# Kernel tuning notes

Measured on AMD Instinct MI355X. Metric: run time of the kernel, lower is better.

Reference implementation:

```python
import jax, jax.numpy as jnp
import numpy as np

B, T, C = 2, 2048, 1024
N_HEAD = 16
HEAD_DIM = C // N_HEAD


def setup_inputs() -> dict:
    key = jax.random.key(0)
    k1, k2, k3 = jax.random.split(key, 3)
    x = jax.random.normal(k1, (B, T, C), dtype=jnp.float32)
    # weights stored as [in, out]; torch Linear computes x @ W.T with weight [out, in]
    W_qkv = jax.random.normal(k2, (C, 3 * C), dtype=jnp.float32) * (1.0 / np.sqrt(C))
    W_proj = jax.random.normal(k3, (C, C), dtype=jnp.float32) * (1.0 / np.sqrt(C))
    return {"x": x, "W_qkv": W_qkv, "W_proj": W_proj}


def reference(x, W_qkv, W_proj):
    Bb, Tt, Cc = x.shape
    qkv = x @ W_qkv                                # [B,T,3C]
    q, k, v = jnp.split(qkv, 3, axis=2)
    # [B,T,H,D] -> [B,H,T,D]
    q = q.reshape(Bb, Tt, N_HEAD, HEAD_DIM).transpose(0, 2, 1, 3)
    k = k.reshape(Bb, Tt, N_HEAD, HEAD_DIM).transpose(0, 2, 1, 3)
    v = v.reshape(Bb, Tt, N_HEAD, HEAD_DIM).transpose(0, 2, 1, 3)
    scale = 1.0 / np.sqrt(HEAD_DIM).astype(np.float32)
    att = jnp.einsum('bhqd,bhkd->bhqk', q, k) * scale   # [B,H,T,T]
    causal = jnp.tril(jnp.ones((Tt, Tt), dtype=bool))
    att = jnp.where(causal[None, None], att, -jnp.inf)
    att = jax.nn.softmax(att, axis=-1)
    y = jnp.einsum('bhqk,bhkd->bhqd', att, v)           # [B,H,T,D]
    y = y.transpose(0, 2, 1, 3).reshape(Bb, Tt, Cc)
    return y @ W_proj
```

## Files before the change

kernel.cpp:

```cpp
#include <hip/hip_runtime.h>
#include <hip/hip_bf16.h>
#include <math.h>


typedef __bf16 bf16_t;
typedef __bf16 bf16x4 __attribute__((ext_vector_type(4)));
typedef __bf16 bf16x8 __attribute__((ext_vector_type(8)));
typedef float  f32x4  __attribute__((ext_vector_type(4)));

#define MFMA16(a, b, c) __builtin_amdgcn_mfma_f32_16x16x32_bf16((a), (b), (c), 0, 0, 0)

#define Bn 2
#define Tn 2048
#define Cn 1024
#define Hn 16
#define Dn 64
#define C3 3072
#define Mn 4096
#define QKW 2048
#define NEG_BIG (-1e30f)
#define SCL2 0.18033688011112042f
#define M2   17.31234049066756f

__device__ __forceinline__ void gload_lds16(const void* g, void* l) {
    __builtin_amdgcn_global_load_lds(
        (const __attribute__((address_space(1))) unsigned int*)g,
        (__attribute__((address_space(3))) unsigned int*)l, 16, 0, 0);
}

__global__ __launch_bounds__(256) void transpose_cvt(const float* __restrict__ in,
                                                     bf16_t* __restrict__ out,
                                                     int K, int N) {
    __shared__ float tile[32][33];
    int n0 = blockIdx.x * 32, k0 = blockIdx.y * 32;
    int tx = threadIdx.x, ty = threadIdx.y;
#pragma unroll
    for (int i = 0; i < 32; i += 8)
        tile[ty + i][tx] = in[(size_t)(k0 + ty + i) * N + n0 + tx];
    __syncthreads();
#pragma unroll
    for (int i = 0; i < 32; i += 8)
        out[(size_t)(n0 + ty + i) * K + k0 + tx] = (bf16_t)tile[tx][ty + i];
}

__global__ __launch_bounds__(256) void cvt_bf16(const float* __restrict__ in,
                                                bf16_t* __restrict__ out) {
    size_t i = ((size_t)blockIdx.x * 256 + threadIdx.x) * 8;
    f32x4 a = *(const f32x4*)(in + i);
    f32x4 b = *(const f32x4*)(in + i + 4);
    bf16x8 r;
    r[0] = (bf16_t)a[0]; r[1] = (bf16_t)a[1]; r[2] = (bf16_t)a[2]; r[3] = (bf16_t)a[3];
    r[4] = (bf16_t)b[0]; r[5] = (bf16_t)b[1]; r[6] = (bf16_t)b[2]; r[7] = (bf16_t)b[3];
    *(bf16x8*)(out + i) = r;
}

template <typename AT, typename CT, int MODE>
__global__ __launch_bounds__(256) void gemm_m97(const AT* __restrict__ A, int lda,
                                                const bf16_t* __restrict__ BT,
                                                CT* __restrict__ Cout, int ldc, int Kd,
                                                bf16_t* __restrict__ qk,
                                                bf16_t* __restrict__ vT) {
    constexpr bool AF32 = (sizeof(AT) == 4);
    __shared__ AT     As[128 * 32];
    __shared__ bf16_t Bs[128 * 32];

    const int tid = threadIdx.x;
    const int w = tid >> 6, lane = tid & 63;
    const int l16 = lane & 15, quad = lane >> 4;
    const int wm = w & 1, wn = w >> 1;
    const int n0 = blockIdx.x * 128;
    const int m0 = blockIdx.y * 128;

    f32x4 zero = {0.f, 0.f, 0.f, 0.f};
    f32x4 acc[4][4];
#pragma unroll
    for (int mb = 0; mb < 4; mb++)
#pragma unroll
        for (int nb = 0; nb < 4; nb++) acc[mb][nb] = zero;

    for (int k = 0; k < Kd; k += 32) {
        __syncthreads();
        if (AF32) {
#pragma unroll
            for (int j = 0; j < 4; j++) {
                int seg = w * 4 + j;
                int r = seg * 8 + (lane >> 3);
                int cc = (lane & 7) ^ (r & 7);
                const float* g = (const float*)A + (size_t)(m0 + r) * lda + k + cc * 4;
                gload_lds16(g, (char*)As + seg * 1024);
            }
        } else {
#pragma unroll
            for (int j = 0; j < 2; j++) {
                int seg = w * 2 + j;
                int r = seg * 16 + (lane >> 2);
                int cc = (lane & 3) ^ (r & 3);
                const bf16_t* g = (const bf16_t*)A + (size_t)(m0 + r) * lda + k + cc * 8;
                gload_lds16(g, (char*)As + seg * 1024);
            }
        }
#pragma unroll
        for (int j = 0; j < 2; j++) {
            int seg = w * 2 + j;
            int r = seg * 16 + (lane >> 2);
            int cc = (lane & 3) ^ (r & 3);
            const bf16_t* g = BT + (size_t)(n0 + r) * Kd + k + cc * 8;
            gload_lds16(g, (char*)Bs + seg * 1024);
        }
        __syncthreads();

        bf16x8 af[4], bf[4];
#pragma unroll
        for (int mb = 0; mb < 4; mb++) {
            int r = wm * 64 + mb * 16 + l16;
            if (AF32) {
                f32x4 x0 = *(const f32x4*)((const char*)As + (r * 8 + ((quad * 2) ^ (r & 7))) * 16);
                f32x4 x1 = *(const f32x4*)((const char*)As + (r * 8 + ((quad * 2 + 1) ^ (r & 7))) * 16);
                bf16x8 t;
                t[0] = (bf16_t)x0[0]; t[1] = (bf16_t)x0[1]; t[2] = (bf16_t)x0[2]; t[3] = (bf16_t)x0[3];
                t[4] = (bf16_t)x1[0]; t[5] = (bf16_t)x1[1]; t[6] = (bf16_t)x1[2]; t[7] = (bf16_t)x1[3];
                af[mb] = t;
            } else {
                af[mb] = *(const bf16x8*)((const char*)As + (r * 4 + (quad ^ (r & 3))) * 16);
            }
        }
#pragma unroll
        for (int nb = 0; nb < 4; nb++) {
            int r = wn * 64 + nb * 16 + l16;
            bf[nb] = *(const bf16x8*)((const char*)Bs + (r * 4 + (quad ^ (r & 3))) * 16);
        }
#pragma unroll
        for (int mb = 0; mb < 4; mb++)
#pragma unroll
            for (int nb = 0; nb < 4; nb++)
                acc[mb][nb] = MFMA16(af[mb], bf[nb], acc[mb][nb]);
    }

#pragma unroll
    for (int mb = 0; mb < 4; mb++)
#pragma unroll
        for (int nb = 0; nb < 4; nb++) {
            const int col = n0 + wn * 64 + nb * 16 + l16;
            const int row0 = m0 + wm * 64 + mb * 16 + quad * 4;
            if (MODE == 0) {
#pragma unroll
                for (int rr = 0; rr < 4; rr++)
                    Cout[(size_t)(row0 + rr) * ldc + col] = (CT)acc[mb][nb][rr];
            } else {
                if (col < 2048) {
#pragma unroll
                    for (int rr = 0; rr < 4; rr++)
                        qk[(size_t)(row0 + rr) * QKW + col] = (bf16_t)acc[mb][nb][rr];
                } else {
                    int hcol = col - 2048;
                    int bb = row0 >> 11, t0 = row0 & 2047;
                    bf16x4 pv;
#pragma unroll
                    for (int rr = 0; rr < 4; rr++) pv[rr] = (bf16_t)acc[mb][nb][rr];
                    *(bf16x4*)(vT + ((size_t)(bb * 1024 + hcol)) * Tn + t0) = pv;
                }
            }
        }
}

__global__ __launch_bounds__(256) void gemm_s(const bf16_t* __restrict__ A, int lda,
                                              const bf16_t* __restrict__ BT,
                                              float* __restrict__ Cout, int ldc, int Kd) {
    __shared__ bf16_t As[64 * 32];
    __shared__ bf16_t Bs[128 * 32];

    const int tid = threadIdx.x;
    const int w = tid >> 6, lane = tid & 63;
    const int l16 = lane & 15, quad = lane >> 4;
    const int wm = w & 1, wn = w >> 1;
    const int n0 = blockIdx.x * 128;
    const int m0 = blockIdx.y * 64;

    f32x4 zero = {0.f, 0.f, 0.f, 0.f};
    f32x4 acc[2][4];
#pragma unroll
    for (int mb = 0; mb < 2; mb++)
#pragma unroll
        for (int nb = 0; nb < 4; nb++) acc[mb][nb] = zero;

    for (int k = 0; k < Kd; k += 32) {
        __syncthreads();
        {
            int r = w * 16 + (lane >> 2);
            int cc = (lane & 3) ^ (r & 3);
            const bf16_t* g = A + (size_t)(m0 + r) * lda + k + cc * 8;
            gload_lds16(g, (char*)As + w * 1024);
        }
#pragma unroll
        for (int j = 0; j < 2; j++) {
            int seg = w * 2 + j;
            int r = seg * 16 + (lane >> 2);
            int cc = (lane & 3) ^ (r & 3);
            const bf16_t* g = BT + (size_t)(n0 + r) * Kd + k + cc * 8;
            gload_lds16(g, (char*)Bs + seg * 1024);
        }
        __syncthreads();

        bf16x8 af[2], bf[4];
#pragma unroll
        for (int mb = 0; mb < 2; mb++) {
            int r = wm * 32 + mb * 16 + l16;
            af[mb] = *(const bf16x8*)((const char*)As + (r * 4 + (quad ^ (r & 3))) * 16);
        }
#pragma unroll
        for (int nb = 0; nb < 4; nb++) {
            int r = wn * 64 + nb * 16 + l16;
            bf[nb] = *(const bf16x8*)((const char*)Bs + (r * 4 + (quad ^ (r & 3))) * 16);
        }
#pragma unroll
        for (int mb = 0; mb < 2; mb++)
#pragma unroll
            for (int nb = 0; nb < 4; nb++)
                acc[mb][nb] = MFMA16(af[mb], bf[nb], acc[mb][nb]);
    }

#pragma unroll
    for (int mb = 0; mb < 2; mb++)
#pragma unroll
        for (int nb = 0; nb < 4; nb++) {
            const int col = n0 + wn * 64 + nb * 16 + l16;
            const int row0 = m0 + wm * 32 + mb * 16 + quad * 4;
#pragma unroll
            for (int rr = 0; rr < 4; rr++)
                Cout[(size_t)(row0 + rr) * ldc + col] = acc[mb][nb][rr];
        }
}

__global__ __launch_bounds__(256) void attn_kernel(bf16_t* __restrict__ qk,
                                                   const bf16_t* __restrict__ vT) {
    const int id = blockIdx.x;
    const int hi = id >> 8;
    const int idx = id & 255;
    const int bh = idx & 31;
    const int xx = idx >> 5;
    const int qt = hi ? (15 - xx) : xx;
    const int b = bh >> 4, h = bh & 15;

    const int tid = threadIdx.x;
    const int wave = tid >> 6, lane = tid & 63;
    const int l16 = lane & 15, quad = lane >> 4;

    __shared__ bf16_t Kb[2][64 * 64];
    __shared__ bf16_t Vb[2][64 * 64];
    __shared__ bf16_t Pl[4][32][72];

    bf16_t* qbase = qk + (size_t)b * Tn * QKW + h * Dn;
    const bf16_t* kbase = qk + (size_t)b * Tn * QKW + Cn + h * Dn;
    const bf16_t* vbase = vT + (size_t)(b * 1024 + h * Dn) * Tn;

    const int q0 = qt * 128 + wave * 32;

    bf16x8 qf[2][2];
#pragma unroll
    for (int g = 0; g < 2; g++)
#pragma unroll
        for (int ks = 0; ks < 2; ks++)
            qf[g][ks] = *(const bf16x8*)(qbase + (size_t)(q0 + g * 16 + l16) * QKW +
                                         ks * 32 + quad * 8);

    bf16x8 ones;
#pragma unroll
    for (int j = 0; j < 8; j++) ones[j] = (bf16_t)1.0f;

    f32x4 zero = {0.f, 0.f, 0.f, 0.f};
    f32x4 o[2][4];
    f32x4 ol[2];
#pragma unroll
    for (int g = 0; g < 2; g++) {
#pragma unroll
        for (int i = 0; i < 4; i++) o[g][i] = zero;
        ol[g] = zero;
    }

    const int nt = 2 * qt + 2;

    const int r8 = lane >> 3;
    const int cc = (lane & 7) ^ r8;
    auto STAGE = [&](int t, int pg) {
        const int key0 = t * 64;
#pragma unroll
        for (int j = 0; j < 2; j++) {
            int seg = wave * 2 + j;
            gload_lds16(kbase + (size_t)(key0 + seg * 8 + r8) * QKW + cc * 8,
                        (char*)&Kb[pg][0] + seg * 1024);
            gload_lds16(vbase + (size_t)(seg * 8 + r8) * Tn + key0 + cc * 8,
                        (char*)&Vb[pg][0] + seg * 1024);
        }
    };

    STAGE(0, 0);
    int cur = 0;

    for (int t = 0; t < nt; ++t) {
        __syncthreads();
        if (t + 1 < nt) STAGE(t + 1, cur ^ 1);

        const char* Kc = (const char*)&Kb[cur][0];
        const char* Vc = (const char*)&Vb[cur][0];

        bf16x8 kf[2][4];
#pragma unroll
        for (int ks = 0; ks < 2; ks++)
#pragma unroll
            for (int nbk = 0; nbk < 4; nbk++) {
                int R = nbk * 16 + l16;
                kf[ks][nbk] = *(const bf16x8*)(Kc + R * 128 +
                                               (((ks * 4 + quad) ^ (R & 7)) << 4));
            }

#pragma unroll
        for (int g = 0; g < 2; g++) {
            f32x4 s[4];
#pragma unroll
            for (int nbk = 0; nbk < 4; nbk++) s[nbk] = zero;
#pragma unroll
            for (int nbk = 0; nbk < 4; nbk++) {
                s[nbk] = MFMA16(kf[0][nbk], qf[g][0], s[nbk]);
                s[nbk] = MFMA16(kf[1][nbk], qf[g][1], s[nbk]);
            }

            if (t >= nt - 2) {
                int q = q0 + g * 16 + l16;
#pragma unroll
                for (int nbk = 0; nbk < 4; nbk++)
#pragma unroll
                    for (int r = 0; r < 4; r++) {
                        int key = t * 64 + nbk * 16 + quad * 4 + r;
                        if (key > q) s[nbk][r] = NEG_BIG;
                    }
            }

#pragma unroll
            for (int nbk = 0; nbk < 4; nbk++) {
                bf16x4 pk;
#pragma unroll
                for (int r = 0; r < 4; r++)
                    pk[r] = (bf16_t)__builtin_exp2f(__builtin_fmaf(s[nbk][r], SCL2, -M2));
                *(bf16x4*)(&Pl[wave][g * 16 + l16][nbk * 16 + quad * 4]) = pk;
            }
        }

        bf16x8 pf[2][2];
#pragma unroll
        for (int g = 0; g < 2; g++)
#pragma unroll
            for (int ks = 0; ks < 2; ks++)
                pf[g][ks] = *(const bf16x8*)(&Pl[wave][g * 16 + l16][ks * 32 + quad * 8]);

#pragma unroll
        for (int ks = 0; ks < 2; ks++) {
#pragma unroll
            for (int nbd = 0; nbd < 4; nbd++) {
                int R = nbd * 16 + l16;
                bf16x8 vf = *(const bf16x8*)(Vc + R * 128 +
                                             (((ks * 4 + quad) ^ (R & 7)) << 4));
                o[0][nbd] = MFMA16(pf[0][ks], vf, o[0][nbd]);
                o[1][nbd] = MFMA16(pf[1][ks], vf, o[1][nbd]);
            }
            ol[0] = MFMA16(pf[0][ks], ones, ol[0]);
            ol[1] = MFMA16(pf[1][ks], ones, ol[1]);
        }

        cur ^= 1;
    }

#pragma unroll
    for (int g = 0; g < 2; g++)
#pragma unroll
        for (int nbd = 0; nbd < 4; nbd++)
#pragma unroll
            for (int r = 0; r < 4; r++) {
                int tq = q0 + g * 16 + quad * 4 + r;
                float val = o[g][nbd][r] / ol[g][r];
                qbase[(size_t)tq * QKW + nbd * 16 + l16] = (bf16_t)val;
            }
}

extern "C" void kernel_launch(void* const* d_in, const int* in_sizes, int n_in,
                              void* d_out, int out_size, void* d_ws, size_t ws_size,
                              hipStream_t stream) {
    const float* x     = (const float*)d_in[0];
    const float* Wqkv  = (const float*)d_in[1];
    const float* Wproj = (const float*)d_in[2];
    float* out = (float*)d_out;

    bf16_t* qk     = (bf16_t*)d_ws;
    bf16_t* vT     = qk + (size_t)Mn * QKW;
    bf16_t* wqkvT  = vT + (size_t)QKW * Tn;
    bf16_t* wprojT = wqkvT + (size_t)C3 * Cn;
    bf16_t* xb     = wprojT + (size_t)Cn * Cn;

    const size_t NEED_XB = ((size_t)Mn * QKW + (size_t)QKW * Tn + (size_t)C3 * Cn +
                            (size_t)Cn * Cn + (size_t)Mn * Cn) * sizeof(bf16_t);

    transpose_cvt<<<dim3(C3 / 32, Cn / 32), dim3(32, 8), 0, stream>>>(Wqkv, wqkvT, Cn, C3);
    transpose_cvt<<<dim3(Cn / 32, Cn / 32), dim3(32, 8), 0, stream>>>(Wproj, wprojT, Cn, Cn);

    if (ws_size >= NEED_XB) {
        cvt_bf16<<<dim3((Mn * Cn) / 2048), 256, 0, stream>>>(x, xb);
        gemm_m97<bf16_t, bf16_t, 1><<<dim3(C3 / 128, Mn / 128), 256, 0, stream>>>(
            xb, Cn, wqkvT, (bf16_t*)nullptr, 0, Cn, qk, vT);
    } else {
        gemm_m97<float, bf16_t, 1><<<dim3(C3 / 128, Mn / 128), 256, 0, stream>>>(
            x, Cn, wqkvT, (bf16_t*)nullptr, 0, Cn, qk, vT);
    }
    attn_kernel<<<dim3(512), 256, 0, stream>>>(qk, vT);
    gemm_s<<<dim3(Cn / 128, Mn / 64), 256, 0, stream>>>(qk, QKW, wprojT, out, Cn, Cn);
}
```

Baseline: 194.7 us.

## Pair complementary 64-row query tiles per block for causal load balance

Each attention block now handles two 64-row query tiles, tile pr and tile 31-pr, over a shared K/V stream. This gives every block the same causal work, replacing the earlier 128-row tiles scheduled high-then-low. Each wave now owns 16 rows per tile instead of 32, and the short tile's MFMAs are skipped once past its diagonal. MFMA sections are wrapped in s_setprio hints. The launch grid must match the new 512-block indexing; the hidden launch code is assumed unchanged at 512 blocks.

```diff
diff --git a/kernel.cpp b/kernel.cpp
--- a/kernel.cpp
+++ b/kernel.cpp
@@ -234,12 +234,12 @@
 __global__ __launch_bounds__(256) void attn_kernel(bf16_t* __restrict__ qk,
                                                    const bf16_t* __restrict__ vT) {
     const int id = blockIdx.x;
-    const int hi = id >> 8;
-    const int idx = id & 255;
-    const int bh = idx & 31;
-    const int xx = idx >> 5;
-    const int qt = hi ? (15 - xx) : xx;
+    const int bh = id & 31;
+    const int pr = id >> 5;
     const int b = bh >> 4, h = bh & 15;
+    const int tA = pr;
+    const int tB = 31 - pr;
+    const int tmax = tB;
 
     const int tid = threadIdx.x;
     const int wave = tid >> 6, lane = tid & 63;
@@ -253,31 +253,26 @@
     const bf16_t* kbase = qk + (size_t)b * Tn * QKW + Cn + h * Dn;
     const bf16_t* vbase = vT + (size_t)(b * 1024 + h * Dn) * Tn;
 
-    const int q0 = qt * 128 + wave * 32;
-
-    bf16x8 qf[2][2];
-#pragma unroll
-    for (int g = 0; g < 2; g++)
-#pragma unroll
-        for (int ks = 0; ks < 2; ks++)
-            qf[g][ks] = *(const bf16x8*)(qbase + (size_t)(q0 + g * 16 + l16) * QKW +
-                                         ks * 32 + quad * 8);
+    const int qA = tA * 64 + wave * 16;
+    const int qB = tB * 64 + wave * 16;
+
+    bf16x8 qfA[2], qfB[2];
+#pragma unroll
+    for (int ks = 0; ks < 2; ks++) {
+        qfA[ks] = *(const bf16x8*)(qbase + (size_t)(qA + l16) * QKW + ks * 32 + quad * 8);
+        qfB[ks] = *(const bf16x8*)(qbase + (size_t)(qB + l16) * QKW + ks * 32 + quad * 8);
+    }
 
     bf16x8 ones;
 #pragma unroll
     for (int j = 0; j < 8; j++) ones[j] = (bf16_t)1.0f;
 
     f32x4 zero = {0.f, 0.f, 0.f, 0.f};
-    f32x4 o[2][4];
-    f32x4 ol[2];
-#pragma unroll
-    for (int g = 0; g < 2; g++) {
-#pragma unroll
-        for (int i = 0; i < 4; i++) o[g][i] = zero;
-        ol[g] = zero;
-    }
-
-    const int nt = 2 * qt + 2;
+    f32x4 oA[4], oB[4];
+    f32x4 olA, olB;
+#pragma unroll
+    for (int i = 0; i < 4; i++) { oA[i] = zero; oB[i] = zero; }
+    olA = zero; olB = zero;
 
     const int r8 = lane >> 3;
     const int cc = (lane & 7) ^ r8;
@@ -296,10 +291,11 @@
     STAGE(0, 0);
     int cur = 0;
 
-    for (int t = 0; t < nt; ++t) {
+    for (int t = 0; t <= tmax; ++t) {
         __syncthreads();
-        if (t + 1 < nt) STAGE(t + 1, cur ^ 1);
-
+        if (t < tmax) STAGE(t + 1, cur ^ 1);
+
+        const bool shp = (t <= tA);
         const char* Kc = (const char*)&Kb[cur][0];
         const char* Vc = (const char*)&Vb[cur][0];
 
@@ -313,19 +309,19 @@
                                                (((ks * 4 + quad) ^ (R & 7)) << 4));
             }
 
-#pragma unroll
-        for (int g = 0; g < 2; g++) {
+        {
             f32x4 s[4];
 #pragma unroll
             for (int nbk = 0; nbk < 4; nbk++) s[nbk] = zero;
+            __builtin_amdgcn_s_setprio(1);
 #pragma unroll
             for (int nbk = 0; nbk < 4; nbk++) {
-                s[nbk] = MFMA16(kf[0][nbk], qf[g][0], s[nbk]);
-                s[nbk] = MFMA16(kf[1][nbk], qf[g][1], s[nbk]);
-            }
-
-            if (t >= nt - 2) {
-                int q = q0 + g * 16 + l16;
+                s[nbk] = MFMA16(kf[0][nbk], qfB[0], s[nbk]);
+                s[nbk] = MFMA16(kf[1][nbk], qfB[1], s[nbk]);
+            }
+            __builtin_amdgcn_s_setprio(0);
+            if (t == tB) {
+                int q = qB + l16;
 #pragma unroll
                 for (int nbk = 0; nbk < 4; nbk++)
 #pragma unroll
@@ -334,24 +330,58 @@
                         if (key > q) s[nbk][r] = NEG_BIG;
                     }
             }
-
 #pragma unroll
             for (int nbk = 0; nbk < 4; nbk++) {
                 bf16x4 pk;
 #pragma unroll
                 for (int r = 0; r < 4; r++)
                     pk[r] = (bf16_t)__builtin_exp2f(__builtin_fmaf(s[nbk][r], SCL2, -M2));
-                *(bf16x4*)(&Pl[wave][g * 16 + l16][nbk * 16 + quad * 4]) = pk;
-            }
-        }
-
-        bf16x8 pf[2][2];
-#pragma unroll
-        for (int g = 0; g < 2; g++)
+                *(bf16x4*)(&Pl[wave][16 + l16][nbk * 16 + quad * 4]) = pk;
+            }
+        }
+
+        if (shp) {
+            f32x4 s[4];
+#pragma unroll
+            for (int nbk = 0; nbk < 4; nbk++) s[nbk] = zero;
+            __builtin_amdgcn_s_setprio(1);
+#pragma unroll
+            for (int nbk = 0; nbk < 4; nbk++) {
+                s[nbk] = MFMA16(kf[0][nbk], qfA[0], s[nbk]);
+                s[nbk] = MFMA16(kf[1][nbk], qfA[1], s[nbk]);
+            }
+            __builtin_amdgcn_s_setprio(0);
+            if (t == tA) {
+                int q = qA + l16;
+#pragma unroll
+                for (int nbk = 0; nbk < 4; nbk++)
+#pragma unroll
+                    for (int r = 0; r < 4; r++) {
+                        int key = t * 64 + nbk * 16 + quad * 4 + r;
+                        if (key > q) s[nbk][r] = NEG_BIG;
+                    }
+            }
+#pragma unroll
+            for (int nbk = 0; nbk < 4; nbk++) {
+                bf16x4 pk;
+#pragma unroll
+                for (int r = 0; r < 4; r++)
+                    pk[r] = (bf16_t)__builtin_exp2f(__builtin_fmaf(s[nbk][r], SCL2, -M2));
+                *(bf16x4*)(&Pl[wave][l16][nbk * 16 + quad * 4]) = pk;
+            }
+        }
+
+        bf16x8 pfB[2], pfA[2];
+#pragma unroll
+        for (int ks = 0; ks < 2; ks++)
+            pfB[ks] = *(const bf16x8*)(&Pl[wave][16 + l16][ks * 32 + quad * 8]);
+        if (shp) {
 #pragma unroll
             for (int ks = 0; ks < 2; ks++)
-                pf[g][ks] = *(const bf16x8*)(&Pl[wave][g * 16 + l16][ks * 32 + quad * 8]);
-
+                pfA[ks] = *(const bf16x8*)(&Pl[wave][l16][ks * 32 + quad * 8]);
+        }
+
+        __builtin_amdgcn_s_setprio(1);
 #pragma unroll
         for (int ks = 0; ks < 2; ks++) {
 #pragma unroll
@@ -359,26 +389,26 @@
                 int R = nbd * 16 + l16;
                 bf16x8 vf = *(const bf16x8*)(Vc + R * 128 +
                                              (((ks * 4 + quad) ^ (R & 7)) << 4));
-                o[0][nbd] = MFMA16(pf[0][ks], vf, o[0][nbd]);
-                o[1][nbd] = MFMA16(pf[1][ks], vf, o[1][nbd]);
-            }
-            ol[0] = MFMA16(pf[0][ks], ones, ol[0]);
-            ol[1] = MFMA16(pf[1][ks], ones, ol[1]);
-        }
+                oB[nbd] = MFMA16(pfB[ks], vf, oB[nbd]);
+                if (shp) oA[nbd] = MFMA16(pfA[ks], vf, oA[nbd]);
+            }
+            olB = MFMA16(pfB[ks], ones, olB);
+            if (shp) olA = MFMA16(pfA[ks], ones, olA);
+        }
+        __builtin_amdgcn_s_setprio(0);
 
         cur ^= 1;
     }
 
 #pragma unroll
-    for (int g = 0; g < 2; g++)
-#pragma unroll
-        for (int nbd = 0; nbd < 4; nbd++)
-#pragma unroll
-            for (int r = 0; r < 4; r++) {
-                int tq = q0 + g * 16 + quad * 4 + r;
-                float val = o[g][nbd][r] / ol[g][r];
-                qbase[(size_t)tq * QKW + nbd * 16 + l16] = (bf16_t)val;
-            }
+    for (int nbd = 0; nbd < 4; nbd++)
+#pragma unroll
+        for (int r = 0; r < 4; r++) {
+            int ta = qA + quad * 4 + r;
+            int tb = qB + quad * 4 + r;
+            qbase[(size_t)ta * QKW + nbd * 16 + l16] = (bf16_t)(oA[nbd][r] / olA[r]);
+            qbase[(size_t)tb * QKW + nbd * 16 + l16] = (bf16_t)(oB[nbd][r] / olB[r]);
+        }
 }
 
 extern "C" void kernel_launch(void* const* d_in, const int* in_sizes, int n_in,
```

Measured after the change: 193.5 us. Within noise of the previous version (-0.6%).
